# Kernel optimization log

Measured on AMD Instinct MI355X. Metric: run time of the kernel, lower is better.

Reference implementation:

```python
import jax, jax.numpy as jnp
import numpy as np

B, S, DM = 2, 1024, 2048          # batch, seq_len, hidden_size
H, HKV, D = 16, 8, 128            # heads, kv heads, head_dim
G = H // HKV                      # kv groups
W = 256                           # bmojo window_size
EPS = 1e-6
SCALE = D ** -0.5                 # softmax_scale (set because qk_norm is used)
NEG = -1e30


def _rmsnorm(x, g):
    # per-head RMSNorm over last dim D
    return x * jax.lax.rsqrt(jnp.mean(x * x, axis=-1, keepdims=True) + EPS) * g


def _rope(x, cos, sin):
    # x: [B,S,H,D]; cos/sin: [B,S,D]
    c = cos[:, :, None, :]
    s = sin[:, :, None, :]
    d2 = x.shape[-1] // 2
    x1, x2 = x[..., :d2], x[..., d2:]
    rot = jnp.concatenate([-x2, x1], axis=-1)
    return x * c + rot * s


def setup_inputs() -> dict:
    key = jax.random.key(0)
    ks = jax.random.split(key, 24)
    std = DM ** -0.5

    def lin_w(k, out_d, in_d):
        return jax.random.normal(k, (out_d, in_d), jnp.float32) * std

    def lin_b(k, out_d):
        return jax.random.normal(k, (out_d,), jnp.float32) * 0.01

    inp = {"hidden_states": jax.random.normal(ks[0], (B, S, DM), jnp.float32)}

    # standard RoPE cos/sin tables (theta=10000), shape [B,S,D]
    pos = jnp.arange(S, dtype=jnp.float32)[:, None]
    inv = 1.0 / (10000.0 ** (jnp.arange(0, D, 2, dtype=jnp.float32) / D))
    emb = jnp.concatenate([pos * inv[None, :]] * 2, axis=-1)  # [S,D]
    inp["cos"] = jnp.broadcast_to(jnp.cos(emb)[None], (B, S, D))
    inp["sin"] = jnp.broadcast_to(jnp.sin(emb)[None], (B, S, D))

    # tied (in-context) projections; attention_bias default -> qkv bias True, o bias False
    inp["Wq"] = lin_w(ks[1], H * D, DM);    inp["bq"] = lin_b(ks[2], H * D)
    inp["Wk"] = lin_w(ks[3], HKV * D, DM);  inp["bk"] = lin_b(ks[4], HKV * D)
    inp["Wv"] = lin_w(ks[5], HKV * D, DM);  inp["bv"] = lin_b(ks[6], HKV * D)
    # untied (fading) projections (tie_attn_weights=False)
    inp["Wq2"] = lin_w(ks[7], H * D, DM);   inp["bq2"] = lin_b(ks[8], H * D)
    inp["Wk2"] = lin_w(ks[9], HKV * D, DM); inp["bk2"] = lin_b(ks[10], HKV * D)
    inp["Wv2"] = lin_w(ks[11], HKV * D, DM); inp["bv2"] = lin_b(ks[12], HKV * D)
    inp["Wo"] = lin_w(ks[13], DM, H * D)
    # QK RMSNorm gammas (near-one so grads are nontrivial)
    inp["gq"] = 1.0 + 0.02 * jax.random.normal(ks[14], (D,), jnp.float32)
    inp["gk"] = 1.0 + 0.02 * jax.random.normal(ks[15], (D,), jnp.float32)
    inp["gq2"] = 1.0 + 0.02 * jax.random.normal(ks[16], (D,), jnp.float32)
    inp["gk2"] = 1.0 + 0.02 * jax.random.normal(ks[17], (D,), jnp.float32)
    return inp


def _qkv(x, cos, sin, Wq, bq, Wk, bk, Wv, bv, gq, gk):
    b, s, _ = x.shape
    q = (x @ Wq.T + bq).reshape(b, s, H, D)
    k = (x @ Wk.T + bk).reshape(b, s, HKV, D)
    v = (x @ Wv.T + bv).reshape(b, s, HKV, D)
    q = _rmsnorm(q, gq)
    k = _rmsnorm(k, gk)
    q = _rope(q, cos, sin)
    k = _rope(k, cos, sin)
    # GQA: expand kv heads to H
    k = jnp.repeat(k, G, axis=2)
    v = jnp.repeat(v, G, axis=2)
    return q, k, v


def reference(hidden_states, cos, sin, Wq, bq, Wk, bk, Wv, bv,
              Wq2, bq2, Wk2, bk2, Wv2, bv2, Wo, gq, gk, gq2, gk2):
    # in-context (tied) and fading (untied) projection paths
    q_ic, k_ic, v_ic = _qkv(hidden_states, cos, sin, Wq, bq, Wk, bk, Wv, bv, gq, gk)
    q_f, k_f, v_f = _qkv(hidden_states, cos, sin, Wq2, bq2, Wk2, bk2, Wv2, bv2, gq2, gk2)

    s_ic = jnp.einsum('bqhd,bkhd->bhqk', q_ic, k_ic) * SCALE
    s_f = jnp.einsum('bqhd,bkhd->bhqk', q_f, k_f) * SCALE

    i = jnp.arange(S)[:, None]
    j = jnp.arange(S)[None, :]
    dij = i - j
    in_window = (dij >= 0) & (dij < W)   # sliding window (window_size-1 lookback + self)
    fading = dij >= W                    # older tokens handled by fading memory

    s_ic = jnp.where(in_window, s_ic, NEG)
    s_f = jnp.where(fading, s_f, NEG)

    # joint softmax over the union of window and fading key sets
    p = jax.nn.softmax(jnp.concatenate([s_ic, s_f], axis=-1), axis=-1)  # [B,H,S,2S]
    p_ic, p_f = p[..., :S], p[..., S:]

    out = jnp.einsum('bhqk,bkhd->bqhd', p_ic, v_ic) \
        + jnp.einsum('bhqk,bkhd->bqhd', p_f, v_f)
    out = out.reshape(B, S, H * D)
    return out @ Wo.T
```

## Files before the change

kernel.cpp:

```cpp
#include <hip/hip_runtime.h>
#include <cstdint>
#include <cstddef>

#define B_    2
#define S_    1024
#define DM_   2048
#define H_    16
#define HKV_  8
#define D_    128
#define W_    256
#define NPROJ 8192
#define MROWS 2048
#define SCALE_ 0.08838834764831845f
#define MNEG  -3.0e38f
#define FIXM  16.0f

typedef float  f32x4  __attribute__((ext_vector_type(4)));
typedef __bf16 bf16x8 __attribute__((ext_vector_type(8)));
typedef __bf16 bf16x4 __attribute__((ext_vector_type(4)));

__device__ __forceinline__ void gload16(const void* g, void* l) {
  __builtin_amdgcn_global_load_lds((const __attribute__((address_space(1))) unsigned int*)g,
                                   (__attribute__((address_space(3))) unsigned int*)l, 16, 0, 0);
}

__global__ __launch_bounds__(256) void cvt_all(
    const float* __restrict__ x,  const float* __restrict__ wq,  const float* __restrict__ wk,
    const float* __restrict__ wv, const float* __restrict__ wq2, const float* __restrict__ wk2,
    const float* __restrict__ wv2,const float* __restrict__ wo,
    const float* __restrict__ bq, const float* __restrict__ bk, const float* __restrict__ bv,
    const float* __restrict__ bq2,const float* __restrict__ bk2,const float* __restrict__ bv2,
    __bf16* __restrict__ xb, __bf16* __restrict__ wall, __bf16* __restrict__ wob,
    float* __restrict__ biasA) {
  const int i = blockIdx.x * 256 + threadIdx.x;
  if (i >= 6293504) return;
  if (i >= 6291456) {
    const int j = i - 6291456, flat = j * 4;
    const int set = flat >> 12, off = flat & 4095;
    const float* bsrc; int boff;
    if (off < 2048)      { bsrc = set ? bq2 : bq; boff = off; }
    else if (off < 3072) { bsrc = set ? bk2 : bk; boff = off - 2048; }
    else                 { bsrc = set ? bv2 : bv; boff = off - 3072; }
    ((f32x4*)biasA)[j] = *(const f32x4*)&bsrc[boff];
    return;
  }
  const float* s; __bf16* d;
  if      (i < 1048576) { s = x   + (size_t)i * 4;              d = xb   + (size_t)i * 4; }
  else if (i < 2097152) { s = wq  + (size_t)(i - 1048576) * 4;  d = wall + (size_t)(i - 1048576) * 4; }
  else if (i < 2621440) { s = wk  + (size_t)(i - 2097152) * 4;  d = wall + 4194304  + (size_t)(i - 2097152) * 4; }
  else if (i < 3145728) { s = wv  + (size_t)(i - 2621440) * 4;  d = wall + 6291456  + (size_t)(i - 2621440) * 4; }
  else if (i < 4194304) { s = wq2 + (size_t)(i - 3145728) * 4;  d = wall + 8388608  + (size_t)(i - 3145728) * 4; }
  else if (i < 4718592) { s = wk2 + (size_t)(i - 4194304) * 4;  d = wall + 12582912 + (size_t)(i - 4194304) * 4; }
  else if (i < 5242880) { s = wv2 + (size_t)(i - 4718592) * 4;  d = wall + 14680064 + (size_t)(i - 4718592) * 4; }
  else                  { s = wo  + (size_t)(i - 5242880) * 4;  d = wob  + (size_t)(i - 5242880) * 4; }
  float4 f = *(const float4*)s;
  bf16x4 o;
  o.x = (__bf16)f.x; o.y = (__bf16)f.y; o.z = (__bf16)f.z; o.w = (__bf16)f.w;
  *(bf16x4*)d = o;
}

template <int MODE>
__global__ __launch_bounds__(512) void gemm8p(const __bf16* __restrict__ A,
                                              const __bf16* __restrict__ Bm,
                                              void* __restrict__ Cv,
                                              const float* __restrict__ bias,
                                              int N, int K, int nxp, int ksplit) {
  __shared__ __align__(16) char lds[131072];
  const int tid = threadIdx.x, lane = tid & 63, wid = tid >> 6;
  const int bid = blockIdx.x, xcd = bid & 7, ii = bid >> 3;
  int x, y, ks;
  if (ksplit == 1) { x = xcd * nxp + (ii % nxp); y = ii / nxp; ks = 0; }
  else             { x = xcd; ks = ii & (ksplit - 1); y = ii / ksplit; }
  const int m0 = y * 256, n0 = x * 256;
  const int kn = K / ksplit, kbeg = ks * kn;
  const int wm = (wid >> 2) * 128, wn = (wid & 3) * 64;
  const int g = lane >> 4, c16 = lane & 15;

  int sRow[8], sCol[8]; bool sA[8];
#pragma unroll
  for (int p = 0; p < 8; ++p) {
    const int o = p * 8192 + tid * 16, ro = o & 32767;
    sA[p]   = o < 32768;
    sRow[p] = ro >> 7;
    sCol[p] = (((ro & 127) ^ ((sRow[p] & 7) << 4))) >> 1;
  }

  auto stage2 = [&](int k0, int buf, int q) {
#pragma unroll
    for (int pp = 0; pp < 2; ++pp) {
      const int p = q * 2 + pp;
      const __bf16* src = sA[p] ? &A [(size_t)(m0 + sRow[p]) * K + k0 + sCol[p]]
                                : &Bm[(size_t)(n0 + sRow[p]) * K + k0 + sCol[p]];
      gload16(src, lds + buf * 65536 + p * 8192 + wid * 1024);
    }
  };
  auto rdA = [&](int buf, int mi, int kk) -> bf16x8 {
    const int r = wm + mi * 16 + c16;
    return *(const bf16x8*)(lds + buf * 65536 + r * 128 + ((kk * 64 + g * 16) ^ ((r & 7) << 4)));
  };
  auto rdB = [&](int buf, int ni, int kk) -> bf16x8 {
    const int r = wn + ni * 16 + c16;
    return *(const bf16x8*)(lds + buf * 65536 + 32768 + r * 128 + ((kk * 64 + g * 16) ^ ((r & 7) << 4)));
  };

  f32x4 acc[8][4] = {};
  const int NT = kn >> 6;

#pragma unroll
  for (int q = 0; q < 4; ++q) stage2(kbeg, 0, q);
  asm volatile("s_waitcnt vmcnt(0)" ::: "memory");
  __builtin_amdgcn_s_barrier();

  for (int t = 0; t < NT; ++t) {
    const int buf = t & 1, k0 = kbeg + t * 64;
    bf16x8 b[4][2];
#pragma unroll
    for (int q = 0; q < 4; ++q) {
      bf16x8 a[2][2];
#pragma unroll
      for (int dm = 0; dm < 2; ++dm)
#pragma unroll
        for (int kk = 0; kk < 2; ++kk) a[dm][kk] = rdA(buf, q * 2 + dm, kk);
      if (q == 0) {
#pragma unroll
        for (int ni = 0; ni < 4; ++ni)
#pragma unroll
          for (int kk = 0; kk < 2; ++kk) b[ni][kk] = rdB(buf, ni, kk);
      }
      if (t + 1 < NT) stage2(k0 + 64, buf ^ 1, q);
      __builtin_amdgcn_s_barrier();
      __builtin_amdgcn_s_setprio(1);
#pragma unroll
      for (int dm = 0; dm < 2; ++dm)
#pragma unroll
        for (int ni = 0; ni < 4; ++ni)
#pragma unroll
          for (int kk = 0; kk < 2; ++kk)
            acc[q * 2 + dm][ni] =
              __builtin_amdgcn_mfma_f32_16x16x32_bf16(a[dm][kk], b[ni][kk], acc[q * 2 + dm][ni], 0, 0, 0);
      __builtin_amdgcn_s_setprio(0);
    }
    if (t + 1 < NT) { asm volatile("s_waitcnt vmcnt(0)" ::: "memory"); }
    __builtin_amdgcn_s_barrier();
  }

#pragma unroll
  for (int mi = 0; mi < 8; ++mi)
#pragma unroll
    for (int ni = 0; ni < 4; ++ni) {
      const int gn = n0 + wn + ni * 16 + c16;
      float bv = 0.f;
      if (MODE == 1) bv = bias[gn];
#pragma unroll
      for (int r = 0; r < 4; ++r) {
        const int gm = m0 + wm + mi * 16 + g * 4 + r;
        if (MODE == 1) ((__bf16*)Cv)[(size_t)gm * N + gn] = (__bf16)(acc[mi][ni][r] + bv);
        else ((float*)Cv)[(size_t)ks * MROWS * N + (size_t)gm * N + gn] = acc[mi][ni][r];
      }
    }
}

__global__ __launch_bounds__(256) void reduce2(const float* __restrict__ a, const float* __restrict__ b,
                                               float* __restrict__ o, int n4) {
  const int i = blockIdx.x * 256 + threadIdx.x;
  if (i >= n4) return;
  ((f32x4*)o)[i] = ((const f32x4*)a)[i] + ((const f32x4*)b)[i];
}

__global__ __launch_bounds__(256) void post_all(const __bf16* __restrict__ proj,
    const float* __restrict__ cosg, const float* __restrict__ sing,
    const float* __restrict__ gq, const float* __restrict__ gk,
    const float* __restrict__ gq2, const float* __restrict__ gk2,
    __bf16* __restrict__ Q0, __bf16* __restrict__ K0,
    __bf16* __restrict__ Q1, __bf16* __restrict__ K1,
    __bf16* __restrict__ Vt0, __bf16* __restrict__ Vt1) {
  __shared__ __bf16 T[64][136];
  const int tid = threadIdx.x;
  if (blockIdx.x < 2048) {
    const int row  = blockIdx.x;
    const int b    = row >> 10;
    const int s    = row & 1023;
    const int lane = tid & 63, wid = tid >> 6;
    const float* cp = cosg + (size_t)row * D_;
    const float* sp = sing + (size_t)row * D_;
    const float c1 = cp[lane], c2 = cp[lane + 64];
    const float s1 = sp[lane], s2 = sp[lane + 64];

    for (int hi = wid; hi < 48; hi += 4) {
      const int  set  = hi >= 24 ? 1 : 0;
      const int  loc  = hi - set * 24;
      const bool isq  = loc < 16;
      const int  head = isq ? loc : loc - 16;
      const __bf16* src = proj + (size_t)row * NPROJ + set * 4096 + (isq ? head * 128 : 2048 + head * 128);
      const float* gv   = set ? (isq ? gq2 : gk2) : (isq ? gq : gk);
      __bf16* dst       = set ? (isq ? Q1 : K1) : (isq ? Q0 : K0);
      const int nheads  = isq ? H_ : HKV_;
      const size_t didx = (((size_t)b * nheads + head) * S_ + s) * D_;
      float x1 = (float)src[lane], x2 = (float)src[lane + 64];
      float ss = x1 * x1 + x2 * x2;
#pragma unroll
      for (int o = 1; o < 64; o <<= 1) ss += __shfl_xor(ss, o);
      const float rr = rsqrtf(ss * (1.f / 128.f) + 1e-6f);
      const float n1 = x1 * rr * gv[lane];
      const float n2 = x2 * rr * gv[lane + 64];
      dst[didx + lane]      = (__bf16)(n1 * c1 - n2 * s1);
      dst[didx + lane + 64] = (__bf16)(n2 * c2 + n1 * s2);
    }
  } else {
    const int bid = blockIdx.x - 2048;
    const int st = bid & 15;
    const int hk = (bid >> 4) & 7;
    const int b  = (bid >> 7) & 1;
    const int sg = bid >> 8;
    const int s0 = st * 64;
    const size_t prow = ((size_t)(b * S_ + s0)) * NPROJ + sg * 4096 + 3072 + hk * 128;
    const int r = tid >> 4, c = (tid & 15) * 8;
#pragma unroll
    for (int pass = 0; pass < 4; ++pass) {
      const int rr = pass * 16 + r;
      *(bf16x8*)&T[rr][c] = *(const bf16x8*)&proj[prow + (size_t)rr * NPROJ + c];
    }
    __syncthreads();
    __bf16* Vt = (sg ? Vt1 : Vt0) + (size_t)(b * HKV_ + hk) * D_ * S_;
    const int d = tid >> 1, half = tid & 1;
#pragma unroll
    for (int q8 = 0; q8 < 4; ++q8) {
      const int sb = half * 32 + q8 * 8;
      bf16x8 v;
#pragma unroll
      for (int k = 0; k < 8; ++k) v[k] = T[sb + k][d];
      *(bf16x8*)&Vt[(size_t)d * S_ + s0 + sb] = v;
    }
  }
}

__global__ __launch_bounds__(256) void attn_fused(
    const __bf16* __restrict__ Q0, const __bf16* __restrict__ K0g, const __bf16* __restrict__ Vt0,
    const __bf16* __restrict__ Q1, const __bf16* __restrict__ K1g, const __bf16* __restrict__ Vt1,
    __bf16* __restrict__ AO) {
  __shared__ __bf16 KsL[2][2][32 * 128];
  __shared__ __bf16 VtL[2][2][128 * 32];
  __shared__ __bf16 Ps[4][16][40];

  const int tid = threadIdx.x, lane = tid & 63, wid = tid >> 6;
  const int bid = blockIdx.x;
  const int xcd = bid & 7, jj = bid >> 3;
  const int combo = xcd * 2 + (jj >> 4);
  const int b = combo >> 3, hk = combo & 7;
  const int h = hk * 2 + ((jj >> 3) & 1);
  const int pq = jj & 7;
  const int qtA = pq, qtB = 15 - pq;
  const int ntA = 2 * qtA + 2;
  const int ntT = 34;

  const int g = lane >> 4, kc = lane & 15;
  const size_t qoff  = (size_t)(b * H_ + h) * S_ * D_;
  const size_t koff  = (size_t)(b * HKV_ + hk) * S_ * D_;
  const size_t vtoff = (size_t)(b * HKV_ + hk) * D_ * S_;

  int kRow[2], kCol[2], vD[2], vJ[2];
#pragma unroll
  for (int p = 0; p < 2; ++p) {
    const int boff = (wid * 2 + p) * 1024 + lane * 16;
    kRow[p] = boff >> 8;
    kCol[p] = ((boff & 255) ^ ((kRow[p] & 7) << 4)) >> 1;
    vD[p]   = boff >> 6;
    vJ[p]   = (boff & 63) >> 1;
  }

  bf16x8 qf0[4], qf1[4];
  auto loadQ = [&](int qw) {
    const int qrow = qw + kc;
#pragma unroll
    for (int c = 0; c < 4; ++c) {
      qf0[c] = *(const bf16x8*)&Q0[qoff + (size_t)qrow * D_ + c * 32 + g * 8];
      qf1[c] = *(const bf16x8*)&Q1[qoff + (size_t)qrow * D_ + c * 32 + g * 8];
    }
  };

  float rs[4];
  f32x4 o[8];
  auto resetS = [&]() {
#pragma unroll
    for (int r = 0; r < 4; ++r) rs[r] = 0.f;
#pragma unroll
    for (int ch = 0; ch < 8; ++ch)
#pragma unroll
      for (int r = 0; r < 4; ++r) o[ch][r] = 0.f;
  };

  auto stage = [&](int qb2, int t, int bufi) {
    const int j0 = t * 32;
    const bool nic = (j0 >= qb2 - 286);
    const bool nf  = (j0 <= qb2 - 193);
#pragma unroll
    for (int p = 0; p < 2; ++p) {
      const int ko = wid * 2048 + p * 1024;
      if (nic) {
        gload16(K0g + koff + (size_t)(j0 + kRow[p]) * D_ + kCol[p], (char*)&KsL[bufi][0][0] + ko);
        gload16(Vt0 + vtoff + (size_t)vD[p] * S_ + j0 + vJ[p],      (char*)&VtL[bufi][0][0] + ko);
      }
      if (nf) {
        gload16(K1g + koff + (size_t)(j0 + kRow[p]) * D_ + kCol[p], (char*)&KsL[bufi][1][0] + ko);
        gload16(Vt1 + vtoff + (size_t)vD[p] * S_ + j0 + vJ[p],      (char*)&VtL[bufi][1][0] + ko);
      }
    }
  };

  auto qk = [&](const __bf16* Kb, const bf16x8 qf[4], f32x4 sv[2]) {
#pragma unroll
    for (int c = 0; c < 4; ++c) {
      const int r0 = kc, r1 = kc + 16;
      const bf16x8 k0f = *(const bf16x8*)((const char*)Kb + r0 * 256 + ((c * 64 + g * 16) ^ ((r0 & 7) << 4)));
      const bf16x8 k1f = *(const bf16x8*)((const char*)Kb + r1 * 256 + ((c * 64 + g * 16) ^ ((r1 & 7) << 4)));
      sv[0] = __builtin_amdgcn_mfma_f32_16x16x32_bf16(qf[c], k0f, sv[0], 0, 0, 0);
      sv[1] = __builtin_amdgcn_mfma_f32_16x16x32_bf16(qf[c], k1f, sv[1], 0, 0, 0);
    }
  };

  auto dopv = [&](const f32x4 sv[2], const __bf16* Vtb) {
#pragma unroll
    for (int nh = 0; nh < 2; ++nh) {
      const int col = kc + nh * 16, c8 = col >> 3, cw = col & 7;
#pragma unroll
      for (int r = 0; r < 4; ++r)
        Ps[wid][g * 4 + r][((c8 ^ g) << 3) + cw] = (__bf16)sv[nh][r];
    }
    asm volatile("s_waitcnt lgkmcnt(0)" ::: "memory");
    const bf16x8 pa = *(const bf16x8*)&Ps[wid][kc][(g ^ (kc >> 2)) << 3];
#pragma unroll
    for (int ch = 0; ch < 8; ++ch) {
      const bf16x8 vb = *(const bf16x8*)&Vtb[(ch * 16 + kc) * 32 + g * 8];
      o[ch] = __builtin_amdgcn_mfma_f32_16x16x32_bf16(pa, vb, o[ch], 0, 0, 0);
    }
  };

  auto writeOut = [&](int qw2) {
    float ell[4];
#pragma unroll
    for (int r = 0; r < 4; ++r) ell[r] = rs[r];
#pragma unroll
    for (int ofs = 1; ofs < 16; ofs <<= 1)
#pragma unroll
      for (int r = 0; r < 4; ++r) ell[r] += __shfl_xor(ell[r], ofs);
#pragma unroll
    for (int r = 0; r < 4; ++r) {
      const float inv = 1.f / ell[r];
      const size_t orow = ((size_t)b * S_ + qw2 + g * 4 + r) * (size_t)(H_ * D_) + h * D_;
#pragma unroll
      for (int ch = 0; ch < 8; ++ch)
        AO[orow + ch * 16 + kc] = (__bf16)(o[ch][r] * inv);
    }
  };

  int qb = qtA * 64, qw = qb + wid * 16;
  loadQ(qw);
  resetS();
  stage(qb, 0, 0);
  asm volatile("s_waitcnt vmcnt(0)" ::: "memory");
  __builtin_amdgcn_s_barrier();
  int cur = 0;

  for (int it = 0; it < ntT; ++it) {
    const int t = (it >= ntA) ? it - ntA : it;
    if (it + 1 < ntT) {
      const bool hN = (it + 1 >= ntA);
      stage(hN ? qtB * 64 : qtA * 64, hN ? it + 1 - ntA : it + 1, cur ^ 1);
    }
    const int j0 = t * 32;
    if (j0 <= qw + 15) {
      const bool w_ic = (j0 >= qw - 286);
      const bool w_f  = (j0 <= qw - 241);

      f32x4 sic[2] = {}, sfd[2] = {};
      if (w_ic) {
        qk(&KsL[cur][0][0], qf0, sic);
#pragma unroll
        for (int nh = 0; nh < 2; ++nh)
#pragma unroll
          for (int r = 0; r < 4; ++r) {
            const int dij = (qw + g * 4 + r) - (j0 + kc + nh * 16);
            const float arg = (dij >= 0 && dij < W_) ? fmaf(sic[nh][r], SCALE_, -FIXM) : MNEG;
            const float p = __expf(arg);
            rs[r] += p; sic[nh][r] = p;
          }
        dopv(sic, &VtL[cur][0][0]);
      }
      if (w_f) {
        qk(&KsL[cur][1][0], qf1, sfd);
#pragma unroll
        for (int nh = 0; nh < 2; ++nh)
#pragma unroll
          for (int r = 0; r < 4; ++r) {
            const int dij = (qw + g * 4 + r) - (j0 + kc + nh * 16);
            const float arg = (dij >= W_) ? fmaf(sfd[nh][r], SCALE_, -FIXM) : MNEG;
            const float p = __expf(arg);
            rs[r] += p; sfd[nh][r] = p;
          }
        dopv(sfd, &VtL[cur][1][0]);
      }
    }
    asm volatile("s_waitcnt vmcnt(0)" ::: "memory");
    __builtin_amdgcn_s_barrier();
    cur ^= 1;

    if (it + 1 == ntA) {
      writeOut(qw);
      resetS();
      qb = qtB * 64; qw = qb + wid * 16;
      loadQ(qw);
    }
  }
  writeOut(qw);
}

extern "C" void kernel_launch(void* const* d_in, const int* in_sizes, int n_in,
                              void* d_out, int out_size, void* d_ws, size_t ws_size,
                              hipStream_t stream) {
  (void)in_sizes; (void)n_in; (void)out_size; (void)ws_size;
  const float* hidden = (const float*)d_in[0];
  const float* cosg   = (const float*)d_in[1];
  const float* sing   = (const float*)d_in[2];
  const float* Wq  = (const float*)d_in[3];
  const float* bq  = (const float*)d_in[4];
  const float* Wk  = (const float*)d_in[5];
  const float* bk  = (const float*)d_in[6];
  const float* Wv  = (const float*)d_in[7];
  const float* bv  = (const float*)d_in[8];
  const float* Wq2 = (const float*)d_in[9];
  const float* bq2 = (const float*)d_in[10];
  const float* Wk2 = (const float*)d_in[11];
  const float* bk2 = (const float*)d_in[12];
  const float* Wv2 = (const float*)d_in[13];
  const float* bv2 = (const float*)d_in[14];
  const float* Wo  = (const float*)d_in[15];
  const float* gq  = (const float*)d_in[16];
  const float* gk  = (const float*)d_in[17];
  const float* gq2 = (const float*)d_in[18];
  const float* gk2 = (const float*)d_in[19];

  char* w = (char*)d_ws;
  __bf16* Xb    = (__bf16*)(w);
  __bf16* Wall  = (__bf16*)(w + 8388608);
  __bf16* Wob   = (__bf16*)(w + 41943040);
  float*  biasA = (float*) (w + 50331648);
  __bf16* proj  = (__bf16*)(w + 50364416);
  __bf16* AO  = Xb;
  __bf16* Q0  = Wall;
  __bf16* Q1  = Wall + 4194304;
  __bf16* K0  = Wall + 8388608;
  __bf16* K1  = Wall + 10485760;
  __bf16* Vt0 = Wall + 12582912;
  __bf16* Vt1 = Wall + 14680064;
  float* part = (float*)proj;

  cvt_all<<<24584, 256, 0, stream>>>(hidden, Wq, Wk, Wv, Wq2, Wk2, Wv2, Wo,
                                     bq, bk, bv, bq2, bk2, bv2,
                                     Xb, Wall, Wob, biasA);
  gemm8p<1><<<256, 512, 0, stream>>>(Xb, Wall, proj, biasA, NPROJ, DM_, 4, 1);
  post_all<<<2560, 256, 0, stream>>>(proj, cosg, sing, gq, gk, gq2, gk2,
                                     Q0, K0, Q1, K1, Vt0, Vt1);
  attn_fused<<<256, 256, 0, stream>>>(Q0, K0, Vt0, Q1, K1, Vt1, AO);
  gemm8p<0><<<128, 512, 0, stream>>>(AO, Wob, part, nullptr, DM_, DM_, 0, 2);
  reduce2<<<4096, 256, 0, stream>>>(part, part + 4194304, (float*)d_out, 1048576);
}
```

Baseline: 185.0 us.

## Reorder GEMM staging chunks and use partial vmcnt waits in pipeline

The GEMM main loop is restructured so that global-to-LDS chunk loads are issued in a reordered sequence (B chunks first, then A chunks interleaved) and the waits use partial vmcnt counts instead of draining all loads. A mid-iteration wait-plus-barrier lets the later A rows of the next tile arrive while the current tile's MFMAs proceed. The aim is to overlap memory latency with compute more tightly and avoid full vmcnt(0) stalls. The risk is subtle ordering bugs: the counts assume per-wave load ordering, and the next-buffer chunks 4-7 are overwritten while other waves may still read them.

```diff
diff --git a/kernel.cpp b/kernel.cpp
--- a/kernel.cpp
+++ b/kernel.cpp
@@ -76,23 +76,13 @@
   const int wm = (wid >> 2) * 128, wn = (wid & 3) * 64;
   const int g = lane >> 4, c16 = lane & 15;
 
-  int sRow[8], sCol[8]; bool sA[8];
-#pragma unroll
-  for (int p = 0; p < 8; ++p) {
-    const int o = p * 8192 + tid * 16, ro = o & 32767;
-    sA[p]   = o < 32768;
-    sRow[p] = ro >> 7;
-    sCol[p] = (((ro & 127) ^ ((sRow[p] & 7) << 4))) >> 1;
-  }
-
-  auto stage2 = [&](int k0, int buf, int q) {
-#pragma unroll
-    for (int pp = 0; pp < 2; ++pp) {
-      const int p = q * 2 + pp;
-      const __bf16* src = sA[p] ? &A [(size_t)(m0 + sRow[p]) * K + k0 + sCol[p]]
-                                : &Bm[(size_t)(n0 + sRow[p]) * K + k0 + sCol[p]];
-      gload16(src, lds + buf * 65536 + p * 8192 + wid * 1024);
-    }
+  const int tR = tid >> 3;
+  const int tC = (((tid & 7) * 16) ^ ((tR & 7) << 4)) >> 1;
+
+  auto stageChunk = [&](int k0, int buf, int c) {
+    const __bf16* src = (c < 4) ? &A [(size_t)(m0 + c * 64 + tR) * K + k0 + tC]
+                                : &Bm[(size_t)(n0 + (c - 4) * 64 + tR) * K + k0 + tC];
+    gload16(src, lds + buf * 65536 + c * 8192 + wid * 1024);
   };
   auto rdA = [&](int buf, int mi, int kk) -> bf16x8 {
     const int r = wm + mi * 16 + c16;
@@ -106,41 +96,93 @@
   f32x4 acc[8][4] = {};
   const int NT = kn >> 6;
 
-#pragma unroll
-  for (int q = 0; q < 4; ++q) stage2(kbeg, 0, q);
-  asm volatile("s_waitcnt vmcnt(0)" ::: "memory");
+  {
+    const int order[8] = {4, 5, 6, 7, 0, 2, 1, 3};
+#pragma unroll
+    for (int i = 0; i < 8; ++i) stageChunk(kbeg, 0, order[i]);
+  }
+  asm volatile("s_waitcnt vmcnt(2)" ::: "memory");
   __builtin_amdgcn_s_barrier();
 
   for (int t = 0; t < NT; ++t) {
-    const int buf = t & 1, k0 = kbeg + t * 64;
+    const int buf = t & 1, k0n = kbeg + (t + 1) * 64;
+    const bool more = (t + 1 < NT);
     bf16x8 b[4][2];
-#pragma unroll
-    for (int q = 0; q < 4; ++q) {
-      bf16x8 a[2][2];
-#pragma unroll
-      for (int dm = 0; dm < 2; ++dm)
-#pragma unroll
-        for (int kk = 0; kk < 2; ++kk) a[dm][kk] = rdA(buf, q * 2 + dm, kk);
-      if (q == 0) {
-#pragma unroll
-        for (int ni = 0; ni < 4; ++ni)
-#pragma unroll
-          for (int kk = 0; kk < 2; ++kk) b[ni][kk] = rdB(buf, ni, kk);
-      }
-      if (t + 1 < NT) stage2(k0 + 64, buf ^ 1, q);
-      __builtin_amdgcn_s_barrier();
-      __builtin_amdgcn_s_setprio(1);
-#pragma unroll
-      for (int dm = 0; dm < 2; ++dm)
-#pragma unroll
-        for (int ni = 0; ni < 4; ++ni)
-#pragma unroll
-          for (int kk = 0; kk < 2; ++kk)
-            acc[q * 2 + dm][ni] =
-              __builtin_amdgcn_mfma_f32_16x16x32_bf16(a[dm][kk], b[ni][kk], acc[q * 2 + dm][ni], 0, 0, 0);
-      __builtin_amdgcn_s_setprio(0);
-    }
-    if (t + 1 < NT) { asm volatile("s_waitcnt vmcnt(0)" ::: "memory"); }
+    bf16x8 a[2][2];
+
+#pragma unroll
+    for (int dm = 0; dm < 2; ++dm)
+#pragma unroll
+      for (int kk = 0; kk < 2; ++kk) a[dm][kk] = rdA(buf, dm, kk);
+#pragma unroll
+    for (int ni = 0; ni < 4; ++ni)
+#pragma unroll
+      for (int kk = 0; kk < 2; ++kk) b[ni][kk] = rdB(buf, ni, kk);
+    if (more) { stageChunk(k0n, buf ^ 1, 4); stageChunk(k0n, buf ^ 1, 5); }
+    __builtin_amdgcn_s_barrier();
+    __builtin_amdgcn_s_setprio(1);
+#pragma unroll
+    for (int dm = 0; dm < 2; ++dm)
+#pragma unroll
+      for (int ni = 0; ni < 4; ++ni)
+#pragma unroll
+        for (int kk = 0; kk < 2; ++kk)
+          acc[dm][ni] = __builtin_amdgcn_mfma_f32_16x16x32_bf16(a[dm][kk], b[ni][kk], acc[dm][ni], 0, 0, 0);
+    __builtin_amdgcn_s_setprio(0);
+
+#pragma unroll
+    for (int dm = 0; dm < 2; ++dm)
+#pragma unroll
+      for (int kk = 0; kk < 2; ++kk) a[dm][kk] = rdA(buf, 2 + dm, kk);
+    if (more) { stageChunk(k0n, buf ^ 1, 6); stageChunk(k0n, buf ^ 1, 7); }
+    __builtin_amdgcn_s_barrier();
+    __builtin_amdgcn_s_setprio(1);
+#pragma unroll
+    for (int dm = 0; dm < 2; ++dm)
+#pragma unroll
+      for (int ni = 0; ni < 4; ++ni)
+#pragma unroll
+        for (int kk = 0; kk < 2; ++kk)
+          acc[2 + dm][ni] = __builtin_amdgcn_mfma_f32_16x16x32_bf16(a[dm][kk], b[ni][kk], acc[2 + dm][ni], 0, 0, 0);
+    __builtin_amdgcn_s_setprio(0);
+
+    if (more) { asm volatile("s_waitcnt vmcnt(4)" ::: "memory"); }
+    else      { asm volatile("s_waitcnt vmcnt(0)" ::: "memory"); }
+    __builtin_amdgcn_s_barrier();
+
+#pragma unroll
+    for (int dm = 0; dm < 2; ++dm)
+#pragma unroll
+      for (int kk = 0; kk < 2; ++kk) a[dm][kk] = rdA(buf, 4 + dm, kk);
+    if (more) { stageChunk(k0n, buf ^ 1, 0); stageChunk(k0n, buf ^ 1, 2); }
+    __builtin_amdgcn_s_barrier();
+    __builtin_amdgcn_s_setprio(1);
+#pragma unroll
+    for (int dm = 0; dm < 2; ++dm)
+#pragma unroll
+      for (int ni = 0; ni < 4; ++ni)
+#pragma unroll
+        for (int kk = 0; kk < 2; ++kk)
+          acc[4 + dm][ni] = __builtin_amdgcn_mfma_f32_16x16x32_bf16(a[dm][kk], b[ni][kk], acc[4 + dm][ni], 0, 0, 0);
+    __builtin_amdgcn_s_setprio(0);
+
+#pragma unroll
+    for (int dm = 0; dm < 2; ++dm)
+#pragma unroll
+      for (int kk = 0; kk < 2; ++kk) a[dm][kk] = rdA(buf, 6 + dm, kk);
+    if (more) { stageChunk(k0n, buf ^ 1, 1); stageChunk(k0n, buf ^ 1, 3); }
+    __builtin_amdgcn_s_barrier();
+    __builtin_amdgcn_s_setprio(1);
+#pragma unroll
+    for (int dm = 0; dm < 2; ++dm)
+#pragma unroll
+      for (int ni = 0; ni < 4; ++ni)
+#pragma unroll
+        for (int kk = 0; kk < 2; ++kk)
+          acc[6 + dm][ni] = __builtin_amdgcn_mfma_f32_16x16x32_bf16(a[dm][kk], b[ni][kk], acc[6 + dm][ni], 0, 0, 0);
+    __builtin_amdgcn_s_setprio(0);
+
+    if (more) { asm volatile("s_waitcnt vmcnt(2)" ::: "memory"); }
     __builtin_amdgcn_s_barrier();
   }
 
```

Measured after the change: 186.7 us. About the same (+0.9%).

## Replace split-K output GEMM and reduce with 128x128-tile direct-write GEMM

Applied to the files above, without the earlier changes.

The output projection previously used 256x256 tiles with a 2-way K split, writing fp32 partials and then running a separate reduce kernel. It now uses a dedicated kernel with 128x128 tiles and 256 threads, launching 256 blocks over the full K and writing the fp32 output directly. This removes the partial-buffer traffic and one kernel launch while keeping parallelism similar. The cost is lower per-block data reuse from the smaller tiles. The QKV GEMM is specialised into its own non-templated kernel with no functional change.

```diff
diff --git a/kernel.cpp b/kernel.cpp
--- a/kernel.cpp
+++ b/kernel.cpp
@@ -59,20 +59,17 @@
   *(bf16x4*)d = o;
 }
 
-template <int MODE>
-__global__ __launch_bounds__(512) void gemm8p(const __bf16* __restrict__ A,
-                                              const __bf16* __restrict__ Bm,
-                                              void* __restrict__ Cv,
-                                              const float* __restrict__ bias,
-                                              int N, int K, int nxp, int ksplit) {
+__global__ __launch_bounds__(512) void gemm_qkv(const __bf16* __restrict__ A,
+                                                const __bf16* __restrict__ Bm,
+                                                __bf16* __restrict__ Cv,
+                                                const float* __restrict__ bias,
+                                                int N, int K, int nxp) {
   __shared__ __align__(16) char lds[131072];
   const int tid = threadIdx.x, lane = tid & 63, wid = tid >> 6;
   const int bid = blockIdx.x, xcd = bid & 7, ii = bid >> 3;
-  int x, y, ks;
-  if (ksplit == 1) { x = xcd * nxp + (ii % nxp); y = ii / nxp; ks = 0; }
-  else             { x = xcd; ks = ii & (ksplit - 1); y = ii / ksplit; }
+  const int x = xcd * nxp + (ii % nxp);
+  const int y = ii / nxp;
   const int m0 = y * 256, n0 = x * 256;
-  const int kn = K / ksplit, kbeg = ks * kn;
   const int wm = (wid >> 2) * 128, wn = (wid & 3) * 64;
   const int g = lane >> 4, c16 = lane & 15;
 
@@ -104,15 +101,15 @@
   };
 
   f32x4 acc[8][4] = {};
-  const int NT = kn >> 6;
-
-#pragma unroll
-  for (int q = 0; q < 4; ++q) stage2(kbeg, 0, q);
+  const int NT = K >> 6;
+
+#pragma unroll
+  for (int q = 0; q < 4; ++q) stage2(0, 0, q);
   asm volatile("s_waitcnt vmcnt(0)" ::: "memory");
   __builtin_amdgcn_s_barrier();
 
   for (int t = 0; t < NT; ++t) {
-    const int buf = t & 1, k0 = kbeg + t * 64;
+    const int buf = t & 1, k0 = t * 64;
     bf16x8 b[4][2];
 #pragma unroll
     for (int q = 0; q < 4; ++q) {
@@ -149,22 +146,92 @@
 #pragma unroll
     for (int ni = 0; ni < 4; ++ni) {
       const int gn = n0 + wn + ni * 16 + c16;
-      float bv = 0.f;
-      if (MODE == 1) bv = bias[gn];
+      const float bv = bias[gn];
 #pragma unroll
       for (int r = 0; r < 4; ++r) {
         const int gm = m0 + wm + mi * 16 + g * 4 + r;
-        if (MODE == 1) ((__bf16*)Cv)[(size_t)gm * N + gn] = (__bf16)(acc[mi][ni][r] + bv);
-        else ((float*)Cv)[(size_t)ks * MROWS * N + (size_t)gm * N + gn] = acc[mi][ni][r];
-      }
-    }
-}
-
-__global__ __launch_bounds__(256) void reduce2(const float* __restrict__ a, const float* __restrict__ b,
-                                               float* __restrict__ o, int n4) {
-  const int i = blockIdx.x * 256 + threadIdx.x;
-  if (i >= n4) return;
-  ((f32x4*)o)[i] = ((const f32x4*)a)[i] + ((const f32x4*)b)[i];
+        Cv[(size_t)gm * N + gn] = (__bf16)(acc[mi][ni][r] + bv);
+      }
+    }
+}
+
+__global__ __launch_bounds__(256) void gemm_out(const __bf16* __restrict__ A,
+                                                const __bf16* __restrict__ Bm,
+                                                float* __restrict__ Cv) {
+  __shared__ __align__(16) char lds[65536];
+  const int tid = threadIdx.x, lane = tid & 63, wid = tid >> 6;
+  const int bid = blockIdx.x, xcd = bid & 7, ii = bid >> 3;
+  const int x = xcd * 2 + (ii & 1);
+  const int y = ii >> 1;
+  const int m0 = y * 128, n0 = x * 128;
+  const int wm = (wid >> 1) * 64, wn = (wid & 1) * 64;
+  const int g = lane >> 4, c16 = lane & 15;
+  const int K = DM_, N = DM_;
+
+  const int tR = tid >> 3;
+  const int tC = (((tid & 7) * 16) ^ ((tR & 7) << 4)) >> 1;
+
+  auto stageP = [&](int k0, int buf, int p) {
+    const __bf16* src = (p < 4) ? &A [(size_t)(m0 + p * 32 + tR) * K + k0 + tC]
+                                : &Bm[(size_t)(n0 + (p - 4) * 32 + tR) * K + k0 + tC];
+    gload16(src, lds + buf * 32768 + p * 4096 + wid * 1024);
+  };
+  auto rdA = [&](int buf, int mi, int kk) -> bf16x8 {
+    const int r = wm + mi * 16 + c16;
+    return *(const bf16x8*)(lds + buf * 32768 + r * 128 + ((kk * 64 + g * 16) ^ ((r & 7) << 4)));
+  };
+  auto rdB = [&](int buf, int ni, int kk) -> bf16x8 {
+    const int r = wn + ni * 16 + c16;
+    return *(const bf16x8*)(lds + buf * 32768 + 16384 + r * 128 + ((kk * 64 + g * 16) ^ ((r & 7) << 4)));
+  };
+
+  f32x4 acc[4][4] = {};
+  const int NT = K >> 6;
+
+#pragma unroll
+  for (int p = 0; p < 8; ++p) stageP(0, 0, p);
+  asm volatile("s_waitcnt vmcnt(0)" ::: "memory");
+  __builtin_amdgcn_s_barrier();
+
+  for (int t = 0; t < NT; ++t) {
+    const int buf = t & 1, k0 = t * 64;
+    bf16x8 b[4][2];
+#pragma unroll
+    for (int q = 0; q < 4; ++q) {
+      bf16x8 a[2];
+#pragma unroll
+      for (int kk = 0; kk < 2; ++kk) a[kk] = rdA(buf, q, kk);
+      if (q == 0) {
+#pragma unroll
+        for (int ni = 0; ni < 4; ++ni)
+#pragma unroll
+          for (int kk = 0; kk < 2; ++kk) b[ni][kk] = rdB(buf, ni, kk);
+      }
+      if (t + 1 < NT) { stageP(k0 + 64, buf ^ 1, q * 2); stageP(k0 + 64, buf ^ 1, q * 2 + 1); }
+      __builtin_amdgcn_s_barrier();
+      __builtin_amdgcn_s_setprio(1);
+#pragma unroll
+      for (int ni = 0; ni < 4; ++ni)
+#pragma unroll
+        for (int kk = 0; kk < 2; ++kk)
+          acc[q][ni] = __builtin_amdgcn_mfma_f32_16x16x32_bf16(a[kk], b[ni][kk], acc[q][ni], 0, 0, 0);
+      __builtin_amdgcn_s_setprio(0);
+    }
+    if (t + 1 < NT) { asm volatile("s_waitcnt vmcnt(0)" ::: "memory"); }
+    __builtin_amdgcn_s_barrier();
+  }
+
+#pragma unroll
+  for (int mi = 0; mi < 4; ++mi)
+#pragma unroll
+    for (int ni = 0; ni < 4; ++ni) {
+      const int gn = n0 + wn + ni * 16 + c16;
+#pragma unroll
+      for (int r = 0; r < 4; ++r) {
+        const int gm = m0 + wm + mi * 16 + g * 4 + r;
+        Cv[(size_t)gm * N + gn] = acc[mi][ni][r];
+      }
+    }
 }
 
 __global__ __launch_bounds__(256) void post_all(const __bf16* __restrict__ proj,
@@ -452,15 +519,13 @@
   __bf16* K1  = Wall + 10485760;
   __bf16* Vt0 = Wall + 12582912;
   __bf16* Vt1 = Wall + 14680064;
-  float* part = (float*)proj;
 
   cvt_all<<<24584, 256, 0, stream>>>(hidden, Wq, Wk, Wv, Wq2, Wk2, Wv2, Wo,
                                      bq, bk, bv, bq2, bk2, bv2,
                                      Xb, Wall, Wob, biasA);
-  gemm8p<1><<<256, 512, 0, stream>>>(Xb, Wall, proj, biasA, NPROJ, DM_, 4, 1);
+  gemm_qkv<<<256, 512, 0, stream>>>(Xb, Wall, proj, biasA, NPROJ, DM_, 4);
   post_all<<<2560, 256, 0, stream>>>(proj, cosg, sing, gq, gk, gq2, gk2,
                                      Q0, K0, Q1, K1, Vt0, Vt1);
   attn_fused<<<256, 256, 0, stream>>>(Q0, K0, Vt0, Q1, K1, Vt1, AO);
-  gemm8p<0><<<128, 512, 0, stream>>>(AO, Wob, part, nullptr, DM_, DM_, 0, 2);
-  reduce2<<<4096, 256, 0, stream>>>(part, part + 4194304, (float*)d_out, 1048576);
-}
+  gemm_out<<<256, 256, 0, stream>>>(AO, Wob, (float*)d_out);
+}
```

New measurement: 177.5 us. 4.1% less time.
